# Optimization experiments

Hardware: AMD Instinct MI355X
Metric: run time of the kernel (lower is better)

Reference implementation:

```python
import jax, jax.numpy as jnp
import numpy as np
import math

D_MODEL = 1024
D_ATTN = 128
D_MID = 128
L = 4096

def setup_inputs() -> dict:
    key = jax.random.key(0)
    ks = jax.random.split(key, 5)
    scale = 1.0 / math.sqrt(D_MODEL)
    return {
        "x": jax.random.normal(ks[0], (L, D_MODEL), jnp.float32),
        "z": jax.random.normal(ks[1], (L, D_MODEL), jnp.float32),
        "Wq": jax.random.normal(ks[2], (D_MODEL, D_ATTN), jnp.float32) * scale,
        "bq": jnp.zeros((D_ATTN,), jnp.float32),
        "Wk": jax.random.normal(ks[3], (D_MODEL, D_ATTN), jnp.float32) * scale,
        "bk": jnp.zeros((D_ATTN,), jnp.float32),
        "Wv": jax.random.normal(ks[4], (D_MODEL, D_MID), jnp.float32) * scale,
        "bv": jnp.zeros((D_MID,), jnp.float32),
    }

def reference(x, z, Wq, bq, Wk, bk, Wv, bv):
    # q: [L_x, d_attn], k: [L_z, d_attn], v: [L_z, d_mid]
    q = x @ Wq + bq
    k = z @ Wk + bk
    v = z @ Wv + bv
    inv_sqrt_d = 1.0 / math.sqrt(D_ATTN)
    s = (q @ k.T) * inv_sqrt_d            # [L_x, L_z]
    y = jax.nn.softmax(s, axis=-1) @ v    # [L_x, d_mid]
    return y
```

## Files before the change

kernel.cpp:

```cpp
#include <hip/hip_runtime.h>
#include <hip/hip_bf16.h>

typedef __attribute__((ext_vector_type(8))) short short8;
typedef __attribute__((ext_vector_type(4))) float f32x4;

#define L_SEQ 4096
#define DM    1024
#define DA    128
#define AZ    16

#define OFF_QB   786432
#define OFF_KF   1835008
#define OFF_VF   2883584
#define OFF_OA   4063232
#define OFF_LA   (OFF_OA + (size_t)AZ * L_SEQ * DA * 4)

__device__ __forceinline__ short f2bf(float f) {
    union { float f; unsigned u; } v; v.f = f;
    unsigned u = v.u;
    u += 0x7FFFu + ((u >> 16) & 1u);
    return (short)(u >> 16);
}

typedef const __attribute__((address_space(1))) void g_void_t;
typedef __attribute__((address_space(3))) void l_void_t;
__device__ __forceinline__ void g2lds16(const void* g, void* l) {
    __builtin_amdgcn_global_load_lds((g_void_t*)g, (l_void_t*)l, 16, 0, 0);
}

__global__ __launch_bounds__(256) void prep_w_kernel(
    const float* __restrict__ Wq, const float* __restrict__ Wk,
    const float* __restrict__ Wv, short8* __restrict__ WTf)
{
    const int m = blockIdx.y, kidx = blockIdx.x;
    const float* __restrict__ W = (m == 0) ? Wq : (m == 1) ? Wk : Wv;
    __shared__ __align__(16) float Ws[32 * 132];
    const int t = threadIdx.x;
#pragma unroll
    for (int i = 0; i < 4; i++) {
        const int u = i * 256 + t;
        const int kk = u >> 5, n4 = (u & 31) * 4;
        *(f32x4*)&Ws[kk * 132 + n4] = *(const f32x4*)&W[(size_t)(kidx * 32 + kk) * DA + n4];
    }
    __syncthreads();
#pragma unroll
    for (int i = 0; i < 2; i++) {
        const int u = i * 256 + t;
        const int nt = u >> 6, lane = u & 63, l16 = lane & 15, quad = lane >> 4;
        short8 fr;
#pragma unroll
        for (int j = 0; j < 8; j++)
            fr[j] = f2bf(Ws[(quad * 8 + j) * 132 + nt * 16 + l16]);
        WTf[((size_t)(m * 32 + kidx) * 8 + nt) * 64 + lane] = fr;
    }
}

__global__ __launch_bounds__(256, 2) void qkv_kernel(
    const float* __restrict__ x, const float* __restrict__ z,
    const char* __restrict__ WTraw,
    const float* __restrict__ bq, const float* __restrict__ bk,
    const float* __restrict__ bv,
    short* __restrict__ qb, short8* __restrict__ kf, short8* __restrict__ vf)
{
    __shared__ __align__(16) char smem[2][16384];

    const int t = threadIdx.x;
    const int w = t >> 6, lane = t & 63;
    const int l16 = lane & 15, quad = lane >> 4;
    const int isKV = blockIdx.y;
    const int row0 = blockIdx.x * 16;
    const int nbytes = isKV ? 16384 : 8192;

    const float* __restrict__ Am = isKV ? z : x;
    const float* ap = Am + (size_t)(row0 + l16) * DM + quad * 8;

    f32x4 acc1[2], acc2[2];
#pragma unroll
    for (int i = 0; i < 2; i++) {
        acc1[i] = (f32x4){0.f, 0.f, 0.f, 0.f};
        acc2[i] = (f32x4){0.f, 0.f, 0.f, 0.f};
    }

    auto stage = [&](int kidx, int b) {
        const char* base1 = WTraw + (size_t)(isKV * 32 + kidx) * 8192;
        const char* base2 = WTraw + (size_t)(64 + kidx) * 8192;
#pragma unroll
        for (int i = 0; i < 4; i++) {
            const int off = i * 4096 + w * 1024;
            if (off < nbytes) {
                const char* src = (off < 8192) ? (base1 + off) : (base2 + (off - 8192));
                g2lds16(src + lane * 16, &smem[b][off]);
            }
        }
    };

    f32x4 c0 = *(const f32x4*)ap,        c1 = *(const f32x4*)(ap + 4);
    f32x4 d0 = *(const f32x4*)(ap + 32), d1 = *(const f32x4*)(ap + 36);

    stage(0, 0);
    __syncthreads();

#pragma unroll 1
    for (int ks = 0; ks < 32; ks++) {
        const int b = ks & 1;
        if (ks + 1 < 32) stage(ks + 1, b ^ 1);

        const int kpf = (ks + 2 < 32) ? ks + 2 : ks;
        f32x4 e0 = *(const f32x4*)(ap + kpf * 32);
        f32x4 e1 = *(const f32x4*)(ap + kpf * 32 + 4);

        short8 afr;
#pragma unroll
        for (int j = 0; j < 4; j++) {
            afr[j]     = f2bf(c0[j]);
            afr[4 + j] = f2bf(c1[j]);
        }

#pragma unroll
        for (int ntl = 0; ntl < 2; ntl++) {
            short8 bfr = *(const short8*)&smem[b][((w * 2 + ntl) * 64 + lane) * 16];
            acc1[ntl] = __builtin_amdgcn_mfma_f32_16x16x32_bf16(afr, bfr, acc1[ntl], 0, 0, 0);
        }
        if (isKV) {
#pragma unroll
            for (int ntl = 0; ntl < 2; ntl++) {
                short8 bfr = *(const short8*)&smem[b][8192 + ((w * 2 + ntl) * 64 + lane) * 16];
                acc2[ntl] = __builtin_amdgcn_mfma_f32_16x16x32_bf16(afr, bfr, acc2[ntl], 0, 0, 0);
            }
        }
        __syncthreads();
        c0 = d0; c1 = d1; d0 = e0; d1 = e1;
    }

    if (!isKV) {
#pragma unroll
        for (int ntl = 0; ntl < 2; ntl++) {
            const int col = w * 32 + ntl * 16 + l16;
            const float bb = bq[col];
#pragma unroll
            for (int r = 0; r < 4; r++)
                qb[(size_t)(row0 + quad * 4 + r) * DA + col] = f2bf(acc1[ntl][r] + bb);
        }
        return;
    }

    short* kT = (short*)&smem[0][0];
    short* vT = kT + 16 * 132;
#pragma unroll
    for (int ntl = 0; ntl < 2; ntl++) {
        const int col = w * 32 + ntl * 16 + l16;
        const float bbk = bk[col], bbv = bv[col];
#pragma unroll
        for (int r = 0; r < 4; r++) {
            const int rl = quad * 4 + r;
            kT[rl * 132 + col] = f2bf(acc1[ntl][r] + bbk);
            vT[rl * 132 + col] = f2bf(acc2[ntl][r] + bbv);
        }
    }
    asm volatile("" ::: "memory");
    __builtin_amdgcn_s_waitcnt(0xc07f);
    asm volatile("" ::: "memory");

    const int kg = blockIdx.x >> 1, nth = blockIdx.x & 1;
    {
        short8 fr;
#pragma unroll
        for (int j = 0; j < 8; j++)
            fr[j] = kT[l16 * 132 + w * 32 + quad * 8 + j];
        kf[((size_t)(kg * 4 + w) * 2 + nth) * 64 + lane] = fr;
    }
    if ((quad >> 1) == nth) {
        const int lr0 = (quad - 2 * nth) * 8;
#pragma unroll
        for (int ntl = 0; ntl < 2; ntl++) {
            const int nt = w * 2 + ntl;
            short8 fr;
#pragma unroll
            for (int j = 0; j < 8; j++)
                fr[j] = vT[(lr0 + j) * 132 + nt * 16 + l16];
            vf[((size_t)kg * 9 + nt) * 64 + lane] = fr;
        }
        if (w == 3) {
            const short one = (short)0x3F80;
            short8 fr;
#pragma unroll
            for (int j = 0; j < 8; j++) fr[j] = (l16 == 0) ? one : (short)0;
            vf[((size_t)kg * 9 + 8) * 64 + lane] = fr;
        }
    }
}

__global__ __launch_bounds__(256, 2) void attn_kernel(
    const short* __restrict__ qb, const char* __restrict__ kfg,
    const char* __restrict__ vfg, float* __restrict__ OA,
    float* __restrict__ lA)
{
    __shared__ __align__(16) char kv[2][17408];
    __shared__ __align__(16) short Ps[4][16 * 40];

    const int t    = threadIdx.x;
    const int wave = t >> 6;
    const int lane = t & 63;
    const int l16  = lane & 15;
    const int quad = lane >> 4;
    const int qr0  = blockIdx.x * 64;
    const int g0   = blockIdx.y * 8;

    auto stage = [&](int g, int b) {
        const char* kb_ = kfg + (size_t)(g0 + g) * 8192;
        const char* vb_ = vfg + (size_t)(g0 + g) * 9216;
#pragma unroll
        for (int i = 0; i < 5; i++) {
            const int off = i * 4096 + wave * 1024;
            if (off < 17408) {
                const char* src = (off < 8192) ? (kb_ + off) : (vb_ + (off - 8192));
                g2lds16(src + lane * 16, &kv[b][off]);
            }
        }
    };

    stage(0, 0);

    short8 af[4];
    const short* qrow = qb + (size_t)(qr0 + wave * 16 + l16) * DA + quad * 8;
#pragma unroll
    for (int ks = 0; ks < 4; ks++)
        af[ks] = *(const short8*)(qrow + ks * 32);

    f32x4 O[9];
#pragma unroll
    for (int i = 0; i < 9; i++) O[i] = (f32x4){0.f, 0.f, 0.f, 0.f};

    const float C = 0.08838834764831845f;
    short* P = &Ps[wave][0];

    __syncthreads();

#pragma unroll 1
    for (int g = 0; g < 8; g++) {
        const int b = g & 1;
        if (g + 1 < 8) stage(g + 1, b ^ 1);

        const char* kb_ = &kv[b][0];
        const char* vb_ = &kv[b][8192];

        f32x4 s0[2];
#pragma unroll
        for (int nh = 0; nh < 2; nh++) s0[nh] = (f32x4){0.f, 0.f, 0.f, 0.f};
#pragma unroll
        for (int nh = 0; nh < 2; nh++)
#pragma unroll
            for (int ks = 0; ks < 4; ks++) {
                short8 bfr = *(const short8*)(kb_ + ((ks * 2 + nh) * 64 + lane) * 16);
                s0[nh] = __builtin_amdgcn_mfma_f32_16x16x32_bf16(af[ks], bfr, s0[nh], 0, 0, 0);
            }

#pragma unroll
        for (int nh = 0; nh < 2; nh++)
#pragma unroll
            for (int r = 0; r < 4; r++)
                P[(quad * 4 + r) * 40 + nh * 16 + l16] = f2bf(__expf(s0[nh][r] * C));
        asm volatile("" ::: "memory");
        __builtin_amdgcn_s_waitcnt(0xc07f);
        asm volatile("" ::: "memory");

        short8 a2 = *(const short8*)&P[l16 * 40 + quad * 8];
#pragma unroll
        for (int nt = 0; nt < 9; nt++) {
            short8 b2 = *(const short8*)(vb_ + (nt * 64 + lane) * 16);
            O[nt] = __builtin_amdgcn_mfma_f32_16x16x32_bf16(a2, b2, O[nt], 0, 0, 0);
        }
        __syncthreads();
    }

    const int rw = qr0 + wave * 16;
    float* Ob = OA + (size_t)blockIdx.y * L_SEQ * DA;
#pragma unroll
    for (int nt = 0; nt < 8; nt++)
#pragma unroll
        for (int r = 0; r < 4; r++)
            Ob[(size_t)(rw + quad * 4 + r) * DA + nt * 16 + l16] = O[nt][r];
    if (l16 == 0) {
        float* lb = lA + (size_t)blockIdx.y * L_SEQ;
#pragma unroll
        for (int r = 0; r < 4; r++)
            lb[rw + quad * 4 + r] = O[8][r];
    }
}

__global__ __launch_bounds__(256) void merge_kernel(
    const float* __restrict__ OA, const float* __restrict__ lA,
    float* __restrict__ out)
{
    const int t = threadIdx.x;
    const int row = blockIdx.x * 16 + (t >> 4);
    const int cg = (t & 15) * 8;

    f32x4 a0 = (f32x4){0.f, 0.f, 0.f, 0.f};
    f32x4 a1 = (f32x4){0.f, 0.f, 0.f, 0.f};
    float lsum = 0.f;
#pragma unroll
    for (int zz = 0; zz < AZ; zz++) {
        const float* p = &OA[((size_t)zz * L_SEQ + row) * DA + cg];
        a0 = a0 + *(const f32x4*)p;
        a1 = a1 + *(const f32x4*)(p + 4);
        lsum += lA[(size_t)zz * L_SEQ + row];
    }
    const float inv = 1.f / lsum;
    f32x4* dst = (f32x4*)&out[(size_t)row * DA + cg];
    dst[0] = a0 * inv;
    dst[1] = a1 * inv;
}

extern "C" void kernel_launch(void* const* d_in, const int* in_sizes, int n_in,
                              void* d_out, int out_size, void* d_ws, size_t ws_size,
                              hipStream_t stream) {
    (void)in_sizes; (void)n_in; (void)out_size; (void)ws_size;
    const float* x  = (const float*)d_in[0];
    const float* z  = (const float*)d_in[1];
    const float* Wq = (const float*)d_in[2];
    const float* bq = (const float*)d_in[3];
    const float* Wk = (const float*)d_in[4];
    const float* bk = (const float*)d_in[5];
    const float* Wv = (const float*)d_in[6];
    const float* bv = (const float*)d_in[7];
    float* out = (float*)d_out;

    short8* WTf = (short8*)d_ws;
    short*  qb  = (short*)((char*)d_ws + OFF_QB);
    short8* kf  = (short8*)((char*)d_ws + OFF_KF);
    short8* vf  = (short8*)((char*)d_ws + OFF_VF);
    float*  OA  = (float*)((char*)d_ws + OFF_OA);
    float*  lA  = (float*)((char*)d_ws + OFF_LA);

    prep_w_kernel<<<dim3(32, 3), 256, 0, stream>>>(Wq, Wk, Wv, WTf);
    qkv_kernel<<<dim3(256, 2), 256, 0, stream>>>(x, z, (const char*)WTf,
                                                 bq, bk, bv, qb, kf, vf);
    attn_kernel<<<dim3(64, AZ), 256, 0, stream>>>(qb, (const char*)kf,
                                                  (const char*)vf, OA, lA);
    merge_kernel<<<256, 256, 0, stream>>>(OA, lA, out);
}
```

Measured before the change: 135.1 us.

## Fuse split-KV merge into attention kernel via last-block atomic counter

```diff
diff --git a/kernel.cpp b/kernel.cpp
--- a/kernel.cpp
+++ b/kernel.cpp
@@ -7,13 +7,14 @@
 #define L_SEQ 4096
 #define DM    1024
 #define DA    128
-#define AZ    16
+#define AZ    8
 
 #define OFF_QB   786432
 #define OFF_KF   1835008
 #define OFF_VF   2883584
 #define OFF_OA   4063232
 #define OFF_LA   (OFF_OA + (size_t)AZ * L_SEQ * DA * 4)
+#define OFF_CNT  (OFF_LA + (size_t)AZ * L_SEQ * 4)
 
 __device__ __forceinline__ short f2bf(float f) {
     union { float f; unsigned u; } v; v.f = f;
@@ -30,9 +31,12 @@
 
 __global__ __launch_bounds__(256) void prep_w_kernel(
     const float* __restrict__ Wq, const float* __restrict__ Wk,
-    const float* __restrict__ Wv, short8* __restrict__ WTf)
+    const float* __restrict__ Wv, short8* __restrict__ WTf,
+    int* __restrict__ cnt)
 {
     const int m = blockIdx.y, kidx = blockIdx.x;
+    if (m == 0 && kidx == 0 && threadIdx.x < 64) cnt[threadIdx.x] = 0;
+
     const float* __restrict__ W = (m == 0) ? Wq : (m == 1) ? Wk : Wv;
     __shared__ __align__(16) float Ws[32 * 132];
     const int t = threadIdx.x;
@@ -193,10 +197,11 @@
 __global__ __launch_bounds__(256, 2) void attn_kernel(
     const short* __restrict__ qb, const char* __restrict__ kfg,
     const char* __restrict__ vfg, float* __restrict__ OA,
-    float* __restrict__ lA)
+    float* __restrict__ lA, float* __restrict__ out, int* __restrict__ cnt)
 {
     __shared__ __align__(16) char kv[2][17408];
     __shared__ __align__(16) short Ps[4][16 * 40];
+    __shared__ int lastFlag;
 
     const int t    = threadIdx.x;
     const int wave = t >> 6;
@@ -204,7 +209,7 @@
     const int l16  = lane & 15;
     const int quad = lane >> 4;
     const int qr0  = blockIdx.x * 64;
-    const int g0   = blockIdx.y * 8;
+    const int g0   = blockIdx.y * 16;
 
     auto stage = [&](int g, int b) {
         const char* kb_ = kfg + (size_t)(g0 + g) * 8192;
@@ -237,9 +242,9 @@
     __syncthreads();
 
 #pragma unroll 1
-    for (int g = 0; g < 8; g++) {
+    for (int g = 0; g < 16; g++) {
         const int b = g & 1;
-        if (g + 1 < 8) stage(g + 1, b ^ 1);
+        if (g + 1 < 16) stage(g + 1, b ^ 1);
 
         const char* kb_ = &kv[b][0];
         const char* vb_ = &kv[b][8192];
@@ -286,30 +291,30 @@
         for (int r = 0; r < 4; r++)
             lb[rw + quad * 4 + r] = O[8][r];
     }
-}
-
-__global__ __launch_bounds__(256) void merge_kernel(
-    const float* __restrict__ OA, const float* __restrict__ lA,
-    float* __restrict__ out)
-{
-    const int t = threadIdx.x;
-    const int row = blockIdx.x * 16 + (t >> 4);
-    const int cg = (t & 15) * 8;
-
-    f32x4 a0 = (f32x4){0.f, 0.f, 0.f, 0.f};
-    f32x4 a1 = (f32x4){0.f, 0.f, 0.f, 0.f};
-    float lsum = 0.f;
-#pragma unroll
-    for (int zz = 0; zz < AZ; zz++) {
-        const float* p = &OA[((size_t)zz * L_SEQ + row) * DA + cg];
-        a0 = a0 + *(const f32x4*)p;
-        a1 = a1 + *(const f32x4*)(p + 4);
-        lsum += lA[(size_t)zz * L_SEQ + row];
-    }
-    const float inv = 1.f / lsum;
-    f32x4* dst = (f32x4*)&out[(size_t)row * DA + cg];
-    dst[0] = a0 * inv;
-    dst[1] = a1 * inv;
+
+    __threadfence();
+    if (t == 0)
+        lastFlag = (atomicAdd(&cnt[blockIdx.x], 1) == AZ - 1);
+    __syncthreads();
+    if (lastFlag) {
+        __threadfence();
+        const int row = qr0 + (t >> 2);
+        const int cg = (t & 3) * 32;
+        f32x4 a[8];
+#pragma unroll
+        for (int j = 0; j < 8; j++) a[j] = (f32x4){0.f, 0.f, 0.f, 0.f};
+        float ls = 0.f;
+        for (int zz = 0; zz < AZ; zz++) {
+            const f32x4* p = (const f32x4*)&OA[((size_t)zz * L_SEQ + row) * DA + cg];
+#pragma unroll
+            for (int j = 0; j < 8; j++) a[j] = a[j] + p[j];
+            ls += lA[(size_t)zz * L_SEQ + row];
+        }
+        const float inv = 1.f / ls;
+        f32x4* dst = (f32x4*)&out[(size_t)row * DA + cg];
+#pragma unroll
+        for (int j = 0; j < 8; j++) dst[j] = a[j] * inv;
+    }
 }
 
 extern "C" void kernel_launch(void* const* d_in, const int* in_sizes, int n_in,
@@ -332,11 +337,11 @@
     short8* vf  = (short8*)((char*)d_ws + OFF_VF);
     float*  OA  = (float*)((char*)d_ws + OFF_OA);
     float*  lA  = (float*)((char*)d_ws + OFF_LA);
-
-    prep_w_kernel<<<dim3(32, 3), 256, 0, stream>>>(Wq, Wk, Wv, WTf);
+    int*    cnt = (int*)((char*)d_ws + OFF_CNT);
+
+    prep_w_kernel<<<dim3(32, 3), 256, 0, stream>>>(Wq, Wk, Wv, WTf, cnt);
     qkv_kernel<<<dim3(256, 2), 256, 0, stream>>>(x, z, (const char*)WTf,
                                                  bq, bk, bv, qb, kf, vf);
     attn_kernel<<<dim3(64, AZ), 256, 0, stream>>>(qb, (const char*)kf,
-                                                  (const char*)vf, OA, lA);
-    merge_kernel<<<256, 256, 0, stream>>>(OA, lA, out);
-}
+                                                  (const char*)vf, OA, lA, out, cnt);
+}
```

New measurement: 198.7 us. +47.1%, slower.
